# Performance work log

Measured on AMD Instinct MI355X. Metric: run time of the kernel, lower is better.

The kernel has to match this reference:

```python
import jax, jax.numpy as jnp
import numpy as np

DIM = 1024
HEADS = 16
DIM_HEAD = 64
INNER = HEADS * DIM_HEAD
SCALE = 8.0  # default scale in plain_cosine_sim_attention
EPS = 1e-5


def setup_inputs() -> dict:
    key = jax.random.key(0)
    ks = jax.random.split(key, 5)
    b, n = 2, 2048
    x = jax.random.normal(ks[0], (b, n, DIM), dtype=jnp.float32)
    ln_w = jnp.ones((DIM,), dtype=jnp.float32)
    ln_b = jnp.zeros((DIM,), dtype=jnp.float32)
    W_qkv = jax.random.normal(ks[1], (DIM, 3 * INNER), dtype=jnp.float32) * (DIM ** -0.5)
    W_out = jax.random.normal(ks[2], (INNER, DIM), dtype=jnp.float32) * (INNER ** -0.5)
    return {"x": x, "ln_w": ln_w, "ln_b": ln_b, "W_qkv": W_qkv, "W_out": W_out}


def _l2norm(t):
    return t / jnp.clip(jnp.linalg.norm(t, axis=-1, keepdims=True), 1e-12)


def reference(x, ln_w, ln_b, W_qkv, W_out):
    b, n, _ = x.shape
    # LayerNorm
    mu = jnp.mean(x, axis=-1, keepdims=True)
    var = jnp.var(x, axis=-1, keepdims=True)
    xn = (x - mu) * jax.lax.rsqrt(var + EPS) * ln_w + ln_b
    # QKV projection (no bias)
    qkv = xn @ W_qkv  # [b, n, 3*inner]
    q, k, v = jnp.split(qkv, 3, axis=-1)
    # [b, n, h*d] -> [b, h, n, d]
    def to_heads(t):
        return t.reshape(b, n, HEADS, DIM_HEAD).transpose(0, 2, 1, 3)
    q, k, v = to_heads(q), to_heads(k), to_heads(v)
    # cosine-sim attention: l2-normalize q, k then scaled dot product
    q = _l2norm(q)
    k = _l2norm(k)
    sim = jnp.einsum('bhid,bhjd->bhij', q, k) * SCALE
    # causal mask
    causal = jnp.tril(jnp.ones((n, n), dtype=bool))
    sim = jnp.where(causal, sim, jnp.finfo(sim.dtype).min)
    attn = jax.nn.softmax(sim, axis=-1)
    o = jnp.einsum('bhij,bhjd->bhid', attn, v)
    # [b, h, n, d] -> [b, n, h*d]
    o = o.transpose(0, 2, 1, 3).reshape(b, n, INNER)
    return o @ W_out
```

## Files before the change

kernel.cpp:

```cpp
#include <hip/hip_runtime.h>
#include <hip/hip_bf16.h>

typedef __attribute__((ext_vector_type(8))) short short8;
typedef __attribute__((ext_vector_type(4))) float floatx4;

__device__ __forceinline__ ushort f2bf(float f) {
    union { __hip_bfloat16 h; ushort u; } cv;
    cv.h = __float2bfloat16(f);
    return cv.u;
}
__device__ __forceinline__ float bf2f(ushort u) {
    union { ushort u; __hip_bfloat16 h; } cv;
    cv.u = u;
    return __bfloat162float(cv.h);
}
__device__ __forceinline__ ushort f2bf_rtz(float f) {
    union { float f; unsigned u; } cv;
    cv.f = f;
    return (ushort)(cv.u >> 16);
}

typedef __attribute__((address_space(1))) void* gas1_t;
typedef __attribute__((address_space(3))) void* las3_t;
__device__ __forceinline__ void cp16(const ushort* g, ushort* l) {
    __builtin_amdgcn_global_load_lds((gas1_t)(unsigned long long)g,
                                     (las3_t)(unsigned long long)l, 16, 0, 0);
}

__global__ __launch_bounds__(256) void transpose_cast(const float* __restrict__ in,
                                                      ushort* __restrict__ out,
                                                      int R, int C) {
    __shared__ float tile[32][33];
    int c0 = blockIdx.x * 32, r0 = blockIdx.y * 32;
    int tx = threadIdx.x, ty = threadIdx.y;
    for (int j = 0; j < 32; j += 8)
        tile[ty + j][tx] = in[(size_t)(r0 + ty + j) * C + c0 + tx];
    __syncthreads();
    for (int j = 0; j < 32; j += 8)
        out[(size_t)(c0 + ty + j) * R + r0 + tx] = f2bf(tile[tx][ty + j]);
}

__global__ __launch_bounds__(256) void ln_kernel(const float* __restrict__ x,
                                                 const float* __restrict__ lw,
                                                 const float* __restrict__ lb,
                                                 ushort* __restrict__ xn) {
    int row = blockIdx.x;
    int tid = threadIdx.x;
    const float4* xr = (const float4*)(x + (size_t)row * 1024);
    float4 v = xr[tid];
    float s = v.x + v.y + v.z + v.w;
    float sq = v.x * v.x + v.y * v.y + v.z * v.z + v.w * v.w;
    for (int off = 32; off; off >>= 1) {
        s += __shfl_xor(s, off);
        sq += __shfl_xor(sq, off);
    }
    __shared__ float ls[4], lq[4];
    int wave = tid >> 6, lane = tid & 63;
    if (lane == 0) { ls[wave] = s; lq[wave] = sq; }
    __syncthreads();
    s = ls[0] + ls[1] + ls[2] + ls[3];
    sq = lq[0] + lq[1] + lq[2] + lq[3];
    float mu = s * (1.0f / 1024.0f);
    float var = sq * (1.0f / 1024.0f) - mu * mu;
    float rs = rsqrtf(var + 1e-5f);
    const float4* wr = (const float4*)lw;
    const float4* br = (const float4*)lb;
    float4 wv = wr[tid], bv = br[tid];
    ushort4 o;
    o.x = f2bf((v.x - mu) * rs * wv.x + bv.x);
    o.y = f2bf((v.y - mu) * rs * wv.y + bv.y);
    o.z = f2bf((v.z - mu) * rs * wv.z + bv.z);
    o.w = f2bf((v.w - mu) * rs * wv.w + bv.w);
    *(ushort4*)&xn[(size_t)row * 1024 + tid * 4] = o;
}

template <typename OutT>
__global__ __launch_bounds__(256) void gemm_bt(const ushort* __restrict__ A,
                                               const ushort* __restrict__ Bt,
                                               OutT* __restrict__ C,
                                               int M, int N, int K) {
    __shared__ ushort As[2][128 * 32];
    __shared__ ushort Bs[2][128 * 32];
    const int tid = threadIdx.x;
    const int wave = tid >> 6, lane = tid & 63;
    const int quad = lane >> 4, l15 = lane & 15;
    const int wm = (wave >> 1) * 64, wn = (wave & 1) * 64;
    const int bm = blockIdx.y * 128, bn = blockIdx.x * 128;

    const int s0 = tid, s1 = tid + 256;
    const int row0 = s0 >> 2, src0 = (s0 & 3) ^ (row0 & 3);
    const int row1 = s1 >> 2, src1 = (s1 & 3) ^ (row1 & 3);

    floatx4 acc[4][4];
    floatx4 z4 = {0.f, 0.f, 0.f, 0.f};
    for (int mi = 0; mi < 4; mi++)
        for (int ni = 0; ni < 4; ni++) acc[mi][ni] = z4;

    const ushort* Ap0 = A + (size_t)(bm + row0) * K + src0 * 8;
    const ushort* Ap1 = A + (size_t)(bm + row1) * K + src1 * 8;
    const ushort* Bp0 = Bt + (size_t)(bn + row0) * K + src0 * 8;
    const ushort* Bp1 = Bt + (size_t)(bn + row1) * K + src1 * 8;

    const int T = K >> 5;
    cp16(Ap0, &As[0][wave * 512]);
    cp16(Ap1, &As[0][2048 + wave * 512]);
    cp16(Bp0, &Bs[0][wave * 512]);
    cp16(Bp1, &Bs[0][2048 + wave * 512]);

    for (int t = 0; t < T; t++) {
        __syncthreads();
        if (t + 1 < T) {
            const int nb = (t + 1) & 1;
            const int k0n = (t + 1) << 5;
            cp16(Ap0 + k0n, &As[nb][wave * 512]);
            cp16(Ap1 + k0n, &As[nb][2048 + wave * 512]);
            cp16(Bp0 + k0n, &Bs[nb][wave * 512]);
            cp16(Bp1 + k0n, &Bs[nb][2048 + wave * 512]);
        }
        const ushort* Ab = As[t & 1];
        const ushort* Bb = Bs[t & 1];
        short8 af[4], bfr[4];
        for (int mi = 0; mi < 4; mi++) {
            int ra = wm + mi * 16 + l15;
            af[mi] = *(const short8*)&Ab[ra * 32 + ((quad ^ (ra & 3)) << 3)];
        }
        for (int ni = 0; ni < 4; ni++) {
            int rb = wn + ni * 16 + l15;
            bfr[ni] = *(const short8*)&Bb[rb * 32 + ((quad ^ (rb & 3)) << 3)];
        }
        for (int mi = 0; mi < 4; mi++)
            for (int ni = 0; ni < 4; ni++)
                acc[mi][ni] = __builtin_amdgcn_mfma_f32_16x16x32_bf16(
                    af[mi], bfr[ni], acc[mi][ni], 0, 0, 0);
    }
    for (int mi = 0; mi < 4; mi++) {
        for (int ni = 0; ni < 4; ni++) {
            for (int r = 0; r < 4; r++) {
                int row = bm + wm + mi * 16 + quad * 4 + r;
                int col = bn + wn + ni * 16 + l15;
                float val = acc[mi][ni][r];
                if constexpr (sizeof(OutT) == 2)
                    ((ushort*)C)[(size_t)row * N + col] = f2bf(val);
                else
                    ((float*)C)[(size_t)row * N + col] = val;
            }
        }
    }
}

__global__ __launch_bounds__(256) void prep(const ushort* __restrict__ qkv,
                                            ushort* __restrict__ Kt,
                                            ushort* __restrict__ Vb,
                                            float* __restrict__ qn,
                                            float* __restrict__ kn) {
    const int nb = blockIdx.x;
    const int h = blockIdx.y;
    const int b = blockIdx.z;
    const int bh = b * 16 + h;
    const int tid = threadIdx.x, wave = tid >> 6, lane = tid & 63;
    __shared__ ushort vt[64][72];

    union S8 { short8 v; ushort u[8]; };
    for (int i = 0; i < 2; i++) {
        int c = tid + i * 256;
        int nl = c >> 3, sg = c & 7;
        S8 vv;
        vv.v = *(const short8*)&qkv[(size_t)(b * 2048 + nb * 64 + nl) * 3072 + 2048 + h * 64 + sg * 8];
        for (int j = 0; j < 8; j++) vt[sg * 8 + j][nl] = vv.u[j];
    }
    __syncthreads();
    for (int i = 0; i < 2; i++) {
        int c = tid + i * 256;
        int d = c >> 3, sg = c & 7;
        *(short8*)&Vb[((size_t)bh * 32 + nb) * 4096 + d * 64 + sg * 8] =
            *(const short8*)&vt[d][sg * 8];
    }

    for (int j = 0; j < 16; j++) {
        int nl = wave * 16 + j;
        size_t rowb = (size_t)(b * 2048 + nb * 64 + nl) * 3072 + h * 64;
        float qv = bf2f(qkv[rowb + lane]);
        float ss = qv * qv;
        for (int off = 32; off; off >>= 1) ss += __shfl_xor(ss, off);
        if (lane == 0) qn[(size_t)bh * 2048 + nb * 64 + nl] = 1.0f / fmaxf(sqrtf(ss), 1e-12f);
        ushort kraw = qkv[rowb + 1024 + lane];
        float kv = bf2f(kraw);
        ss = kv * kv;
        for (int off = 32; off; off >>= 1) ss += __shfl_xor(ss, off);
        if (lane == 0) kn[(size_t)bh * 2048 + nb * 64 + nl] = 1.0f / fmaxf(sqrtf(ss), 1e-12f);
        Kt[((size_t)bh * 2048 + nb * 64 + nl) * 64 + lane] = kraw;
    }
}

#define LOG2E8 11.541560327111707f

__global__ __launch_bounds__(256) void flash_attn(const ushort* __restrict__ qkv,
                                                  const float* __restrict__ qn,
                                                  const float* __restrict__ kn,
                                                  const ushort* __restrict__ Kt,
                                                  const ushort* __restrict__ Vb,
                                                  ushort* __restrict__ O) {
    const int pairi = blockIdx.x;
    const int h = blockIdx.y;
    const int b = blockIdx.z;
    const int bh = b * 16 + h;
    const int tid = threadIdx.x;
    const int wave = tid >> 6, lane = tid & 63;
    const int quad = lane >> 4, l15 = lane & 15;

    __shared__ ushort Ks[2][64 * 64];
    __shared__ ushort Vs[2][64 * 64];
    __shared__ ushort Ps[4][16 * 72];

    const int ch0 = tid, ch1 = tid + 256;
    const int r0 = ch0 >> 3, sg0 = (ch0 & 7) ^ (r0 & 7);
    const int r1 = ch1 >> 3, sg1 = (ch1 & 7) ^ (r1 & 7);

    const ushort* Kp0 = Kt + ((size_t)bh * 2048 + r0) * 64 + sg0 * 8;
    const ushort* Kp1 = Kt + ((size_t)bh * 2048 + r1) * 64 + sg1 * 8;
    const ushort* Vp0 = Vb + (size_t)bh * 131072 + r0 * 64 + sg0 * 8;
    const ushort* Vp1 = Vb + (size_t)bh * 131072 + r1 * 64 + sg1 * 8;

    const float* knb = kn + (size_t)bh * 2048;
    floatx4 z4 = {0.f, 0.f, 0.f, 0.f};

    for (int pass = 0; pass < 2; pass++) {
        const int st = pass ? (31 - pairi) : pairi;
        const int q0 = st * 64;

        const ushort* Qp = qkv + (size_t)(b * 2048 + q0 + wave * 16 + l15) * 3072 + h * 64;
        short8 qf0 = *(const short8*)(Qp + quad * 8);
        short8 qf1 = *(const short8*)(Qp + 32 + quad * 8);
        float a_r[4];
        for (int r = 0; r < 4; r++)
            a_r[r] = LOG2E8 * qn[(size_t)bh * 2048 + q0 + wave * 16 + quad * 4 + r];

        float rs_acc[4] = {0.f, 0.f, 0.f, 0.f};
        floatx4 o_acc[4];
        for (int ni = 0; ni < 4; ni++) o_acc[ni] = z4;

        __syncthreads();
        cp16(Kp0, &Ks[0][wave * 512]);
        cp16(Kp1, &Ks[0][2048 + wave * 512]);
        cp16(Vp0, &Vs[0][wave * 512]);
        cp16(Vp1, &Vs[0][2048 + wave * 512]);

        for (int kt = 0; kt <= st; kt++) {
            const int kv0 = kt * 64;
            __syncthreads();
            if (kt < st) {
                const int nb2 = (kt + 1) & 1;
                const size_t to = (size_t)(kt + 1) * 4096;
                cp16(Kp0 + to, &Ks[nb2][wave * 512]);
                cp16(Kp1 + to, &Ks[nb2][2048 + wave * 512]);
                cp16(Vp0 + to, &Vs[nb2][wave * 512]);
                cp16(Vp1 + to, &Vs[nb2][2048 + wave * 512]);
            }
            const ushort* Kb = Ks[kt & 1];
            const ushort* Vb_ = Vs[kt & 1];

            floatx4 s_acc[4];
            for (int ni = 0; ni < 4; ni++) s_acc[ni] = z4;
            for (int ni = 0; ni < 4; ni++) {
                int rb = ni * 16 + l15;
                short8 kf0 = *(const short8*)&Kb[rb * 64 + ((quad ^ (rb & 7)) << 3)];
                short8 kf1 = *(const short8*)&Kb[rb * 64 + (((quad + 4) ^ (rb & 7)) << 3)];
                s_acc[ni] = __builtin_amdgcn_mfma_f32_16x16x32_bf16(qf0, kf0, s_acc[ni], 0, 0, 0);
                s_acc[ni] = __builtin_amdgcn_mfma_f32_16x16x32_bf16(qf1, kf1, s_acc[ni], 0, 0, 0);
            }

            const bool diag = (kt == st);
            for (int ni = 0; ni < 4; ni++) {
                const int col_loc = ni * 16 + l15;
                const float knv = knb[kv0 + col_loc];
                for (int r = 0; r < 4; r++) {
                    float e = __builtin_amdgcn_exp2f(
                        fmaf(s_acc[ni][r] * knv, a_r[r], -LOG2E8));
                    if (diag && col_loc > wave * 16 + quad * 4 + r) e = 0.f;
                    rs_acc[r] += e;
                    Ps[wave][(quad * 4 + r) * 72 + col_loc] = f2bf_rtz(e);
                }
            }

            short8 pa0 = *(const short8*)&Ps[wave][l15 * 72 + quad * 8];
            short8 pa1 = *(const short8*)&Ps[wave][l15 * 72 + 32 + quad * 8];
            for (int ni = 0; ni < 4; ni++) {
                int rv = ni * 16 + l15;
                short8 v0 = *(const short8*)&Vb_[rv * 64 + ((quad ^ (rv & 7)) << 3)];
                short8 v1 = *(const short8*)&Vb_[rv * 64 + (((quad + 4) ^ (rv & 7)) << 3)];
                o_acc[ni] = __builtin_amdgcn_mfma_f32_16x16x32_bf16(pa0, v0, o_acc[ni], 0, 0, 0);
                o_acc[ni] = __builtin_amdgcn_mfma_f32_16x16x32_bf16(pa1, v1, o_acc[ni], 0, 0, 0);
            }
        }

        for (int r = 0; r < 4; r++) {
            float rs = rs_acc[r];
            for (int off = 1; off < 16; off <<= 1) rs += __shfl_xor(rs, off);
            float inv = 1.0f / rs;
            int grow = q0 + wave * 16 + quad * 4 + r;
            size_t rowbase = ((size_t)b * 2048 + grow) * 1024 + h * 64;
            for (int ni = 0; ni < 4; ni++)
                O[rowbase + ni * 16 + l15] = f2bf(o_acc[ni][r] * inv);
        }
    }
}

extern "C" void kernel_launch(void* const* d_in, const int* in_sizes, int n_in,
                              void* d_out, int out_size, void* d_ws, size_t ws_size,
                              hipStream_t stream) {
    const float* x = (const float*)d_in[0];
    const float* ln_w = (const float*)d_in[1];
    const float* ln_b = (const float*)d_in[2];
    const float* W_qkv = (const float*)d_in[3];
    const float* W_out = (const float*)d_in[4];

    char* w = (char*)d_ws;
    ushort* xn    = (ushort*)(w);
    ushort* WqkvT = (ushort*)(w + (8ull << 20));
    ushort* WoutT = (ushort*)(w + (14ull << 20));
    ushort* qkv   = (ushort*)(w + (16ull << 20));
    ushort* Vb    = (ushort*)(w + (40ull << 20));
    float*  qn    = (float*)(w + (48ull << 20));
    float*  kn    = (float*)(w + (49ull << 20));
    ushort* obuf  = (ushort*)(w + (50ull << 20));
    ushort* Kt    = (ushort*)(w + (58ull << 20));

    transpose_cast<<<dim3(96, 32), dim3(32, 8), 0, stream>>>(W_qkv, WqkvT, 1024, 3072);
    transpose_cast<<<dim3(32, 32), dim3(32, 8), 0, stream>>>(W_out, WoutT, 1024, 1024);
    ln_kernel<<<4096, 256, 0, stream>>>(x, ln_w, ln_b, xn);
    gemm_bt<ushort><<<dim3(24, 32), 256, 0, stream>>>(xn, WqkvT, qkv, 4096, 3072, 1024);
    prep<<<dim3(32, 16, 2), 256, 0, stream>>>(qkv, Kt, Vb, qn, kn);
    flash_attn<<<dim3(16, 16, 2), 256, 0, stream>>>(qkv, qn, kn, Kt, Vb, obuf);
    gemm_bt<float><<<dim3(8, 32), 256, 0, stream>>>(obuf, WoutT, (float*)d_out, 4096, 1024, 1024);
}
```

Baseline: 209.1 us.

## Pre-normalize Q and K in prep and remap attention blocks per XCD

The prep kernel now writes l2-normalized Q and K in bf16 into head-contiguous buffers, so the attention inner loop no longer loads per-key norms or multiplies by per-row scales before exp2. Q is also read from a compact per-head layout instead of the strided qkv buffer. The attention grid is flattened and remapped so each XCD handles four complete (batch, head) pairs, which should improve L2 locality for K/V. Rounding the normalized vectors to bf16 slightly changes precision compared with applying fp32 norms after the dot product.

Result: faster. 196.3 us (-6.1%).

```diff
diff --git a/kernel.cpp b/kernel.cpp
--- a/kernel.cpp
+++ b/kernel.cpp
@@ -149,10 +149,9 @@
 }
 
 __global__ __launch_bounds__(256) void prep(const ushort* __restrict__ qkv,
+                                            ushort* __restrict__ Qt,
                                             ushort* __restrict__ Kt,
-                                            ushort* __restrict__ Vb,
-                                            float* __restrict__ qn,
-                                            float* __restrict__ kn) {
+                                            ushort* __restrict__ Vb) {
     const int nb = blockIdx.x;
     const int h = blockIdx.y;
     const int b = blockIdx.z;
@@ -179,31 +178,33 @@
     for (int j = 0; j < 16; j++) {
         int nl = wave * 16 + j;
         size_t rowb = (size_t)(b * 2048 + nb * 64 + nl) * 3072 + h * 64;
+        size_t orow = ((size_t)bh * 2048 + nb * 64 + nl) * 64;
+
         float qv = bf2f(qkv[rowb + lane]);
         float ss = qv * qv;
         for (int off = 32; off; off >>= 1) ss += __shfl_xor(ss, off);
-        if (lane == 0) qn[(size_t)bh * 2048 + nb * 64 + nl] = 1.0f / fmaxf(sqrtf(ss), 1e-12f);
-        ushort kraw = qkv[rowb + 1024 + lane];
-        float kv = bf2f(kraw);
+        float inv = 1.0f / fmaxf(sqrtf(ss), 1e-12f);
+        Qt[orow + lane] = f2bf(qv * inv);
+
+        float kv = bf2f(qkv[rowb + 1024 + lane]);
         ss = kv * kv;
         for (int off = 32; off; off >>= 1) ss += __shfl_xor(ss, off);
-        if (lane == 0) kn[(size_t)bh * 2048 + nb * 64 + nl] = 1.0f / fmaxf(sqrtf(ss), 1e-12f);
-        Kt[((size_t)bh * 2048 + nb * 64 + nl) * 64 + lane] = kraw;
+        inv = 1.0f / fmaxf(sqrtf(ss), 1e-12f);
+        Kt[orow + lane] = f2bf(kv * inv);
     }
 }
 
 #define LOG2E8 11.541560327111707f
 
-__global__ __launch_bounds__(256) void flash_attn(const ushort* __restrict__ qkv,
-                                                  const float* __restrict__ qn,
-                                                  const float* __restrict__ kn,
+__global__ __launch_bounds__(256) void flash_attn(const ushort* __restrict__ Qt,
                                                   const ushort* __restrict__ Kt,
                                                   const ushort* __restrict__ Vb,
                                                   ushort* __restrict__ O) {
-    const int pairi = blockIdx.x;
-    const int h = blockIdx.y;
-    const int b = blockIdx.z;
-    const int bh = b * 16 + h;
+    const int id = blockIdx.x;
+    const int xcd = id & 7, slot = id >> 3;
+    const int bh = xcd * 4 + (slot >> 4);
+    const int pairi = slot & 15;
+    const int b = bh >> 4, h = bh & 15;
     const int tid = threadIdx.x;
     const int wave = tid >> 6, lane = tid & 63;
     const int quad = lane >> 4, l15 = lane & 15;
@@ -221,19 +222,15 @@
     const ushort* Vp0 = Vb + (size_t)bh * 131072 + r0 * 64 + sg0 * 8;
     const ushort* Vp1 = Vb + (size_t)bh * 131072 + r1 * 64 + sg1 * 8;
 
-    const float* knb = kn + (size_t)bh * 2048;
     floatx4 z4 = {0.f, 0.f, 0.f, 0.f};
 
     for (int pass = 0; pass < 2; pass++) {
         const int st = pass ? (31 - pairi) : pairi;
         const int q0 = st * 64;
 
-        const ushort* Qp = qkv + (size_t)(b * 2048 + q0 + wave * 16 + l15) * 3072 + h * 64;
+        const ushort* Qp = Qt + ((size_t)bh * 2048 + q0 + wave * 16 + l15) * 64;
         short8 qf0 = *(const short8*)(Qp + quad * 8);
         short8 qf1 = *(const short8*)(Qp + 32 + quad * 8);
-        float a_r[4];
-        for (int r = 0; r < 4; r++)
-            a_r[r] = LOG2E8 * qn[(size_t)bh * 2048 + q0 + wave * 16 + quad * 4 + r];
 
         float rs_acc[4] = {0.f, 0.f, 0.f, 0.f};
         floatx4 o_acc[4];
@@ -246,7 +243,6 @@
         cp16(Vp1, &Vs[0][2048 + wave * 512]);
 
         for (int kt = 0; kt <= st; kt++) {
-            const int kv0 = kt * 64;
             __syncthreads();
             if (kt < st) {
                 const int nb2 = (kt + 1) & 1;
@@ -272,10 +268,9 @@
             const bool diag = (kt == st);
             for (int ni = 0; ni < 4; ni++) {
                 const int col_loc = ni * 16 + l15;
-                const float knv = knb[kv0 + col_loc];
                 for (int r = 0; r < 4; r++) {
                     float e = __builtin_amdgcn_exp2f(
-                        fmaf(s_acc[ni][r] * knv, a_r[r], -LOG2E8));
+                        fmaf(s_acc[ni][r], LOG2E8, -LOG2E8));
                     if (diag && col_loc > wave * 16 + quad * 4 + r) e = 0.f;
                     rs_acc[r] += e;
                     Ps[wave][(quad * 4 + r) * 72 + col_loc] = f2bf_rtz(e);
@@ -320,16 +315,15 @@
     ushort* WoutT = (ushort*)(w + (14ull << 20));
     ushort* qkv   = (ushort*)(w + (16ull << 20));
     ushort* Vb    = (ushort*)(w + (40ull << 20));
-    float*  qn    = (float*)(w + (48ull << 20));
-    float*  kn    = (float*)(w + (49ull << 20));
-    ushort* obuf  = (ushort*)(w + (50ull << 20));
-    ushort* Kt    = (ushort*)(w + (58ull << 20));
+    ushort* Qt    = (ushort*)(w + (48ull << 20));
+    ushort* obuf  = (ushort*)(w + (56ull << 20));
+    ushort* Kt    = (ushort*)(w + (64ull << 20));
 
     transpose_cast<<<dim3(96, 32), dim3(32, 8), 0, stream>>>(W_qkv, WqkvT, 1024, 3072);
     transpose_cast<<<dim3(32, 32), dim3(32, 8), 0, stream>>>(W_out, WoutT, 1024, 1024);
     ln_kernel<<<4096, 256, 0, stream>>>(x, ln_w, ln_b, xn);
     gemm_bt<ushort><<<dim3(24, 32), 256, 0, stream>>>(xn, WqkvT, qkv, 4096, 3072, 1024);
-    prep<<<dim3(32, 16, 2), 256, 0, stream>>>(qkv, Kt, Vb, qn, kn);
-    flash_attn<<<dim3(16, 16, 2), 256, 0, stream>>>(qkv, qn, kn, Kt, Vb, obuf);
+    prep<<<dim3(32, 16, 2), 256, 0, stream>>>(qkv, Qt, Kt, Vb);
+    flash_attn<<<512, 256, 0, stream>>>(Qt, Kt, Vb, obuf);
     gemm_bt<float><<<dim3(8, 32), 256, 0, stream>>>(obuf, WoutT, (float*)d_out, 4096, 1024, 1024);
 }
```
